# Kernel tuning notes

Hardware: AMD Instinct MI355X
Metric: run time of the kernel (lower is better)

## Reference

```python
import jax, jax.numpy as jnp
import numpy as np

EMB = 1024
HEADS = 16
HEAD = EMB // HEADS
B, S = 4, 1024


def setup_inputs() -> dict:
    key = jax.random.key(0)
    ks = jax.random.split(key, 8)
    glorot = lambda k, shp: jax.random.normal(k, shp, jnp.float32) * np.sqrt(2.0 / (shp[-2] + shp[-1]))
    return {
        "inputs_for_keys": jax.random.normal(ks[0], (B, S, EMB), jnp.float32),
        "inputs_for_values": jax.random.normal(ks[1], (B, S, EMB), jnp.float32),
        "inputs_for_queries": jax.random.normal(ks[2], (B, S, EMB), jnp.float32),
        "Wk": glorot(ks[3], (HEADS, EMB, HEAD)),
        "Wv": glorot(ks[4], (HEADS, EMB, HEAD)),
        "Wq": glorot(ks[5], (HEADS, EMB, HEAD)),
        "Wo": glorot(ks[6], (EMB, EMB)),
        "bo": jnp.zeros((EMB,), jnp.float32),
    }


def reference(inputs_for_keys, inputs_for_values, inputs_for_queries, Wk, Wv, Wq, Wo, bo):
    # Batched equivalent of the per-head loop: project all heads at once.
    K = jnp.einsum("bse,hed->bhsd", inputs_for_keys, Wk)
    V = jnp.einsum("bse,hed->bhsd", inputs_for_values, Wv)
    Q = jnp.einsum("bse,hed->bhsd", inputs_for_queries, Wq)
    s_keys = K.shape[2]
    s_q = Q.shape[2]
    # causal mask: -inf strictly above diagonal (original: np.triu(ones*-inf, k=1))
    mask = jnp.where(jnp.triu(jnp.ones((s_q, s_keys), bool), k=1), -jnp.inf, 0.0).astype(jnp.float32)
    logits = jnp.einsum("bhqd,bhkd->bhqk", Q, K)
    # FAITHFUL quirk: original divides (logits + mask) by sqrt(window_size_keys)
    scores = jax.nn.softmax((logits + mask) / np.sqrt(s_keys), axis=-1)
    ctx = jnp.einsum("bhqk,bhkd->bhqd", scores, V)  # [B,H,Sq,Dh]
    # concat heads along last dim (head order matches loop order)
    concat = ctx.transpose(0, 2, 1, 3).reshape(ctx.shape[0], s_q, -1)  # [B,Sq,E]
    return jax.nn.relu(concat @ Wo + bo)
```

## Files before the change

### kernel.cpp

```cpp
#include <hip/hip_runtime.h>
#include <hip/hip_bf16.h>

typedef unsigned short u16;
typedef unsigned int   u32;
typedef __attribute__((ext_vector_type(4))) float f32x4;
typedef __attribute__((ext_vector_type(8))) short bf16x8;

#define EMB   1024
#define SEQ   1024
#define HEADS 16
#define DH    64
#define BATCH 4
#define BH    64
#define BS    4096
#define LDP   72
#define NEG_BIG (-1.0e30f)

__device__ __forceinline__ float b2f(u16 u){ return __uint_as_float(((u32)u) << 16); }
__device__ __forceinline__ u16 f2b(float f){
    u32 u = __float_as_uint(f);
    u32 r = u + 0x7fffu + ((u >> 16) & 1u);
    return (u16)(r >> 16);
}
__device__ __forceinline__ void zero4(f32x4& v){ v[0]=0.f; v[1]=0.f; v[2]=0.f; v[3]=0.f; }
__device__ __forceinline__ ushort4 pk4(float a, float b, float c, float d){
    ushort4 p; p.x = f2b(a); p.y = f2b(b); p.z = f2b(c); p.w = f2b(d); return p;
}

__device__ __forceinline__ u16* tptr(u16* base, int row, int col ){
    const int phys = ((col >> 3) ^ (row & 7));
    return base + row * 64 + (phys << 3);
}

__device__ __forceinline__ void dot2_f32(const float* __restrict__ x,
                                         const float* __restrict__ w, const int ws,
                                         float& a0, float& a1)
{
    float s0 = 0.f, s1 = 0.f;
    for (int e = 0; e < EMB; e += 4) {
        const float4 xv = *(const float4*)(x + e);
        const float2 w0 = *(const float2*)(w + (size_t)(e + 0) * ws);
        const float2 w1 = *(const float2*)(w + (size_t)(e + 1) * ws);
        const float2 w2 = *(const float2*)(w + (size_t)(e + 2) * ws);
        const float2 w3 = *(const float2*)(w + (size_t)(e + 3) * ws);
        s0 += xv.x * w0.x; s1 += xv.x * w0.y;
        s0 += xv.y * w1.x; s1 += xv.y * w1.y;
        s0 += xv.z * w2.x; s1 += xv.z * w2.y;
        s0 += xv.w * w3.x; s1 += xv.w * w3.y;
    }
    a0 = s0; a1 = s1;
}


__global__ __launch_bounds__(256) void convert_x(
    const float* __restrict__ Xk, const float* __restrict__ Xv, const float* __restrict__ Xq,
    u16* __restrict__ XB)
{
    const int which = blockIdx.y;
    const float* __restrict__ src = (which == 0) ? Xk : (which == 1) ? Xv : Xq;
    const size_t off = (size_t)blockIdx.x * 1024 + threadIdx.x * 4;
    const float4 v = *(const float4*)(src + off);
    *(ushort4*)(XB + (size_t)which * 4194304 + off) = pk4(v.x, v.y, v.z, v.w);
}

__global__ __launch_bounds__(256) void transpose_w(
    const float* __restrict__ Wk, const float* __restrict__ Wv, const float* __restrict__ Wq,
    const float* __restrict__ Wo, u16* __restrict__ WT, u16* __restrict__ WoT)
{
    __shared__ u16 T[64][LDP];
    const int which = blockIdx.y;
    const int bx = blockIdx.x, t = threadIdx.x;

    if (which < 3) {
        const float* __restrict__ W = (which == 0) ? Wk : (which == 1) ? Wv : Wq;
        const int h = bx >> 4, e0 = (bx & 15) * 64;
        #pragma unroll
        for (int i = 0; i < 16; ++i) {
            const int idx = i * 256 + t;
            const int e = idx >> 6, d = idx & 63;
            T[d][e] = f2b(W[(size_t)h * (EMB * DH) + (size_t)(e0 + e) * DH + d]);
        }
        __syncthreads();
        u16* dstb = WT + (size_t)which * (EMB * EMB / 16) * 16;
        #pragma unroll
        for (int i = 0; i < 2; ++i) {
            const int idx = i * 256 + t;
            const int d = idx >> 3, e8 = (idx & 7) * 8;
            *(bf16x8*)(dstb + (size_t)(h * 64 + d) * EMB + e0 + e8) = *(const bf16x8*)&T[d][e8];
        }
    } else {
        const int j0 = (bx >> 4) * 64, e0 = (bx & 15) * 64;
        #pragma unroll
        for (int i = 0; i < 16; ++i) {
            const int idx = i * 256 + t;
            const int e = idx >> 6, d = idx & 63;
            T[d][e] = f2b(Wo[(size_t)(e0 + e) * EMB + j0 + d]);
        }
        __syncthreads();
        #pragma unroll
        for (int i = 0; i < 2; ++i) {
            const int idx = i * 256 + t;
            const int d = idx >> 3, e8 = (idx & 7) * 8;
            *(bf16x8*)(WoT + (size_t)(j0 + d) * EMB + e0 + e8) = *(const bf16x8*)&T[d][e8];
        }
    }
}

template<int MODE>
__global__ __launch_bounds__(256) void gemm128(
    const u16* __restrict__ XB, const u16* __restrict__ WT,
    u16* __restrict__ Qw, u16* __restrict__ Kw, u16* __restrict__ Vt,
    const float* __restrict__ bo, float* __restrict__ OUT)
{
    __shared__ u16 As[128 * 64];
    __shared__ u16 Bs[128 * 64];

    const int t = threadIdx.x;
    const int wave = t >> 6, lane = t & 63;
    const int quad = lane >> 4, l16 = lane & 15;
    const int wrow = wave >> 1, wcol = wave & 1;
    const int m0 = blockIdx.x * 128;
    const int n0 = blockIdx.y * 128;
    const int which = blockIdx.z;

    const u16* __restrict__ Ag = (MODE == 0) ? XB + (size_t)which * 4194304 : XB;
    const u16* __restrict__ Bg = (MODE == 0) ? WT + (size_t)which * 1048576 : WT;

    f32x4 acc[4][4];
    #pragma unroll
    for (int mi = 0; mi < 4; ++mi)
        #pragma unroll
        for (int ni = 0; ni < 4; ++ni) zero4(acc[mi][ni]);

    for (int k0 = 0; k0 < EMB; k0 += 64) {
        bf16x8 abuf[4], bbuf[4];
        #pragma unroll
        for (int i = 0; i < 4; ++i) {
            const int c = i * 256 + t;
            const int row = c >> 3, col8 = (c & 7) * 8;
            abuf[i] = *(const bf16x8*)(Ag + (size_t)(m0 + row) * EMB + k0 + col8);
            bbuf[i] = *(const bf16x8*)(Bg + (size_t)(n0 + row) * EMB + k0 + col8);
        }
        #pragma unroll
        for (int i = 0; i < 4; ++i) {
            const int c = i * 256 + t;
            const int row = c >> 3, col8 = (c & 7) * 8;
            *(bf16x8*)tptr(As, row, col8) = abuf[i];
            *(bf16x8*)tptr(Bs, row, col8) = bbuf[i];
        }
        __syncthreads();

        #pragma unroll
        for (int kb = 0; kb < 2; ++kb) {
            bf16x8 af[4], bf[4];
            #pragma unroll
            for (int mi = 0; mi < 4; ++mi)
                af[mi] = *(const bf16x8*)tptr(As, wrow * 64 + mi * 16 + l16, kb * 32 + quad * 8);
            #pragma unroll
            for (int ni = 0; ni < 4; ++ni)
                bf[ni] = *(const bf16x8*)tptr(Bs, wcol * 64 + ni * 16 + l16, kb * 32 + quad * 8);
            #pragma unroll
            for (int mi = 0; mi < 4; ++mi)
                #pragma unroll
                for (int ni = 0; ni < 4; ++ni)
                    acc[mi][ni] = __builtin_amdgcn_mfma_f32_16x16x32_bf16(af[mi], bf[ni], acc[mi][ni], 0, 0, 0);
        }
        __syncthreads();
    }

    #pragma unroll
    for (int mi = 0; mi < 4; ++mi) {
        const int r = m0 + wrow * 64 + mi * 16 + quad * 4;
        #pragma unroll
        for (int ni = 0; ni < 4; ++ni) {
            const int j = n0 + wcol * 64 + ni * 16 + l16;
            if (MODE == 1) {
                const float bias = bo[j];
                #pragma unroll
                for (int reg = 0; reg < 4; ++reg) {
                    float v = acc[mi][ni][reg] + bias;
                    if (v < 0.f) v = 0.f;
                    OUT[(size_t)(r + reg) * EMB + j] = v;
                }
            } else {
                const int h = j >> 6, d = j & 63;
                const int b = r >> 10, s = r & (SEQ - 1);
                const int bh = b * HEADS + h;
                if (which == 1) {
                    *(ushort4*)(Vt + ((size_t)bh * DH + d) * SEQ + s) =
                        pk4(acc[mi][ni][0], acc[mi][ni][1], acc[mi][ni][2], acc[mi][ni][3]);
                } else {
                    u16* dst = (which == 0) ? Kw : Qw;
                    #pragma unroll
                    for (int reg = 0; reg < 4; ++reg)
                        dst[((size_t)bh * SEQ + s + reg) * DH + d] = f2b(acc[mi][ni][reg]);
                }
            }
        }
    }
}


__global__ __launch_bounds__(256) void qkv_proj_mfma(
    const float* __restrict__ Xk, const float* __restrict__ Xv, const float* __restrict__ Xq,
    const float* __restrict__ Wk, const float* __restrict__ Wv, const float* __restrict__ Wq,
    u16* __restrict__ Kw, u16* __restrict__ Vw, u16* __restrict__ Qw)
{
    __shared__ u16 As[128][LDP];
    __shared__ u16 Bs[64][LDP];

    const int which = blockIdx.z;
    const float* __restrict__ X = (which == 0) ? Xk : (which == 1) ? Xv : Xq;
    const float* __restrict__ W = (which == 0) ? Wk : (which == 1) ? Wv : Wq;

    const int h    = blockIdx.y;
    const int m0   = blockIdx.x * 128;
    const int t    = threadIdx.x;
    const int wave = t >> 6, lane = t & 63;
    const int quad = lane >> 4, l16 = lane & 15;

    f32x4 acc[2][4];
    #pragma unroll
    for (int mi = 0; mi < 2; ++mi)
        #pragma unroll
        for (int ni = 0; ni < 4; ++ni) zero4(acc[mi][ni]);

    const size_t wbase = (size_t)h * EMB * DH;
    for (int k0 = 0; k0 < EMB; k0 += 64) {
        #pragma unroll
        for (int i = 0; i < 8; ++i) {
            const int idx = i * 256 + t;
            const int r = idx >> 4, c4 = (idx & 15) * 4;
            const float4 v = *(const float4*)(X + (size_t)(m0 + r) * EMB + k0 + c4);
            *(ushort4*)&As[r][c4] = pk4(v.x, v.y, v.z, v.w);
        }
        #pragma unroll
        for (int i = 0; i < 4; ++i) {
            const int d  = t & 63;
            const int e0 = (t >> 6) * 4 + i * 16;
            const float v0 = W[wbase + (size_t)(k0 + e0 + 0) * DH + d];
            const float v1 = W[wbase + (size_t)(k0 + e0 + 1) * DH + d];
            const float v2 = W[wbase + (size_t)(k0 + e0 + 2) * DH + d];
            const float v3 = W[wbase + (size_t)(k0 + e0 + 3) * DH + d];
            *(ushort4*)&Bs[d][e0] = pk4(v0, v1, v2, v3);
        }
        __syncthreads();

        #pragma unroll
        for (int kb = 0; kb < 2; ++kb) {
            bf16x8 bfr[4];
            #pragma unroll
            for (int ni = 0; ni < 4; ++ni)
                bfr[ni] = *(const bf16x8*)&Bs[ni * 16 + l16][kb * 32 + quad * 8];
            #pragma unroll
            for (int mi = 0; mi < 2; ++mi) {
                const bf16x8 af = *(const bf16x8*)&As[wave * 32 + mi * 16 + l16][kb * 32 + quad * 8];
                #pragma unroll
                for (int ni = 0; ni < 4; ++ni)
                    acc[mi][ni] = __builtin_amdgcn_mfma_f32_16x16x32_bf16(af, bfr[ni], acc[mi][ni], 0, 0, 0);
            }
        }
        __syncthreads();
    }

    const int b  = m0 >> 10;
    const int bh = b * HEADS + h;
    u16* __restrict__ RowDst = (which == 0) ? Kw : Qw;
    #pragma unroll
    for (int mi = 0; mi < 2; ++mi) {
        const int s_base = (m0 & (SEQ - 1)) + wave * 32 + mi * 16 + quad * 4;
        #pragma unroll
        for (int ni = 0; ni < 4; ++ni) {
            const int d = ni * 16 + l16;
            if (which != 1) {
                #pragma unroll
                for (int reg = 0; reg < 4; ++reg)
                    RowDst[((size_t)bh * SEQ + s_base + reg) * DH + d] = f2b(acc[mi][ni][reg]);
            } else {
                *(ushort4*)(Vw + ((size_t)bh * DH + d) * SEQ + s_base) =
                    pk4(acc[mi][ni][0], acc[mi][ni][1], acc[mi][ni][2], acc[mi][ni][3]);
            }
        }
    }
}

template<bool QWS, bool TOWS>
__global__ __launch_bounds__(256) void attn_flash(
    const float* __restrict__ Xq, const float* __restrict__ Wq,
    const u16* __restrict__ Qg, const u16* __restrict__ Kg, const u16* __restrict__ Vg,
    u16* __restrict__ CTXb, float* __restrict__ CTXf)
{
    __shared__ u16 Qs[64][LDP];
    union KVU {
        struct { u16 Ks[64][LDP]; u16 Vt[64][LDP]; } kv;
        struct { u16 Xs[64][LDP]; u16 WT[64][LDP]; } pr;
    };
    __shared__ KVU uu;
    __shared__ u16 Ps[64][LDP];

    const int t    = threadIdx.x;
    const int wave = t >> 6, lane = t & 63;
    const int quad = lane >> 4, l16 = lane & 15;
    const int qt = blockIdx.x, bh = blockIdx.y;
    const int b  = bh >> 4, h = bh & (HEADS - 1);
    const int q0 = qt * 64;

    if (QWS) {
        #pragma unroll
        for (int i = 0; i < 4; ++i) {
            const int idx = i * 256 + t;
            const int r = idx >> 4, c4 = (idx & 15) * 4;
            *(ushort4*)&Qs[r][c4] = *(const ushort4*)(Qg + ((size_t)bh * SEQ + q0 + r) * DH + c4);
        }
    } else {
        f32x4 qacc[4];
        #pragma unroll
        for (int ni = 0; ni < 4; ++ni) zero4(qacc[ni]);
        const size_t wbase = (size_t)h * EMB * DH;
        for (int k0 = 0; k0 < EMB; k0 += 64) {
            #pragma unroll
            for (int i = 0; i < 4; ++i) {
                const int idx = i * 256 + t;
                const int r = idx >> 4, c4 = (idx & 15) * 4;
                const float4 v = *(const float4*)(Xq + (size_t)(b * SEQ + q0 + r) * EMB + k0 + c4);
                *(ushort4*)&uu.pr.Xs[r][c4] = pk4(v.x, v.y, v.z, v.w);
            }
            #pragma unroll
            for (int i = 0; i < 4; ++i) {
                const int d  = t & 63;
                const int e0 = (t >> 6) * 4 + i * 16;
                const float v0 = Wq[wbase + (size_t)(k0 + e0 + 0) * DH + d];
                const float v1 = Wq[wbase + (size_t)(k0 + e0 + 1) * DH + d];
                const float v2 = Wq[wbase + (size_t)(k0 + e0 + 2) * DH + d];
                const float v3 = Wq[wbase + (size_t)(k0 + e0 + 3) * DH + d];
                *(ushort4*)&uu.pr.WT[d][e0] = pk4(v0, v1, v2, v3);
            }
            __syncthreads();
            #pragma unroll
            for (int kb = 0; kb < 2; ++kb) {
                const bf16x8 af = *(const bf16x8*)&uu.pr.Xs[wave * 16 + l16][kb * 32 + quad * 8];
                #pragma unroll
                for (int ni = 0; ni < 4; ++ni) {
                    const bf16x8 bf = *(const bf16x8*)&uu.pr.WT[ni * 16 + l16][kb * 32 + quad * 8];
                    qacc[ni] = __builtin_amdgcn_mfma_f32_16x16x32_bf16(af, bf, qacc[ni], 0, 0, 0);
                }
            }
            __syncthreads();
        }
        #pragma unroll
        for (int ni = 0; ni < 4; ++ni)
            #pragma unroll
            for (int reg = 0; reg < 4; ++reg)
                Qs[wave * 16 + quad * 4 + reg][ni * 16 + l16] = f2b(qacc[ni][reg]);
    }

    float m[4], l[4];
    #pragma unroll
    for (int reg = 0; reg < 4; ++reg) { m[reg] = NEG_BIG; l[reg] = 0.f; }
    f32x4 oacc[4];
    #pragma unroll
    for (int ni = 0; ni < 4; ++ni) zero4(oacc[ni]);
    __syncthreads();

    for (int c = 0; c <= qt; ++c) {
        const int k0 = c * 64;

        #pragma unroll
        for (int i = 0; i < 4; ++i) {
            const int idx = i * 256 + t;
            const int r = idx >> 4, c4 = (idx & 15) * 4;
            *(ushort4*)&uu.kv.Ks[r][c4] = *(const ushort4*)(Kg + ((size_t)bh * SEQ + k0 + r) * DH + c4);
        }
        #pragma unroll
        for (int i = 0; i < 4; ++i) {
            const int idx = i * 256 + t;
            const int r = idx >> 4, c4 = (idx & 15) * 4;
            *(ushort4*)&uu.kv.Vt[r][c4] = *(const ushort4*)(Vg + ((size_t)bh * DH + r) * SEQ + k0 + c4);
        }
        __syncthreads();

        f32x4 sacc[4];
        #pragma unroll
        for (int ni = 0; ni < 4; ++ni) zero4(sacc[ni]);
        #pragma unroll
        for (int kb = 0; kb < 2; ++kb) {
            const bf16x8 af = *(const bf16x8*)&Qs[wave * 16 + l16][kb * 32 + quad * 8];
            #pragma unroll
            for (int ni = 0; ni < 4; ++ni) {
                const bf16x8 bf = *(const bf16x8*)&uu.kv.Ks[ni * 16 + l16][kb * 32 + quad * 8];
                sacc[ni] = __builtin_amdgcn_mfma_f32_16x16x32_bf16(af, bf, sacc[ni], 0, 0, 0);
            }
        }

        const bool diag = (c == qt);
        #pragma unroll
        for (int reg = 0; reg < 4; ++reg) {
            const int rloc = quad * 4 + reg;
            float sv[4];
            #pragma unroll
            for (int ni = 0; ni < 4; ++ni) {
                float s = sacc[ni][reg] * 0.03125f;
                if (diag && (ni * 16 + l16 > wave * 16 + rloc)) s = NEG_BIG;
                sv[ni] = s;
            }
            float mx = fmaxf(fmaxf(sv[0], sv[1]), fmaxf(sv[2], sv[3]));
            mx = fmaxf(mx, m[reg]);
            #pragma unroll
            for (int off = 1; off < 16; off <<= 1) mx = fmaxf(mx, __shfl_xor(mx, off));
            const float alpha = __expf(m[reg] - mx);
            float rs = 0.f;
            #pragma unroll
            for (int ni = 0; ni < 4; ++ni) {
                const float p = __expf(sv[ni] - mx);
                Ps[wave * 16 + rloc][ni * 16 + l16] = f2b(p);
                rs += p;
            }
            #pragma unroll
            for (int off = 1; off < 16; off <<= 1) rs += __shfl_xor(rs, off);
            l[reg] = l[reg] * alpha + rs;
            m[reg] = mx;
            #pragma unroll
            for (int ni = 0; ni < 4; ++ni) oacc[ni][reg] *= alpha;
        }
        __syncthreads();

        #pragma unroll
        for (int kb = 0; kb < 2; ++kb) {
            const bf16x8 af = *(const bf16x8*)&Ps[wave * 16 + l16][kb * 32 + quad * 8];
            #pragma unroll
            for (int ni = 0; ni < 4; ++ni) {
                const bf16x8 bf = *(const bf16x8*)&uu.kv.Vt[ni * 16 + l16][kb * 32 + quad * 8];
                oacc[ni] = __builtin_amdgcn_mfma_f32_16x16x32_bf16(af, bf, oacc[ni], 0, 0, 0);
            }
        }
        __syncthreads();
    }

    float il[4];
    #pragma unroll
    for (int reg = 0; reg < 4; ++reg) il[reg] = 1.f / l[reg];
    #pragma unroll
    for (int ni = 0; ni < 4; ++ni) {
        const int d = ni * 16 + l16;
        #pragma unroll
        for (int reg = 0; reg < 4; ++reg) {
            const int q = wave * 16 + quad * 4 + reg;
            const float val = oacc[ni][reg] * il[reg];
            const size_t off = ((size_t)(b * SEQ + q0 + q)) * EMB + h * DH + d;
            if (TOWS) CTXb[off] = f2b(val);
            else      CTXf[off] = val;
        }
    }
}

__global__ __launch_bounds__(256) void out_proj_mfma(
    const u16* __restrict__ CTXb, const float* __restrict__ Wo,
    const float* __restrict__ bo, float* __restrict__ OUT)
{
    __shared__ u16 As[128][LDP];
    __shared__ u16 Bs[64][LDP];

    const int m0 = blockIdx.x * 128;
    const int n0 = blockIdx.y * 64;
    const int t = threadIdx.x;
    const int wave = t >> 6, lane = t & 63;
    const int quad = lane >> 4, l16 = lane & 15;

    f32x4 acc[2][4];
    #pragma unroll
    for (int mi = 0; mi < 2; ++mi)
        #pragma unroll
        for (int ni = 0; ni < 4; ++ni) zero4(acc[mi][ni]);

    for (int k0 = 0; k0 < EMB; k0 += 64) {
        #pragma unroll
        for (int i = 0; i < 8; ++i) {
            const int idx = i * 256 + t;
            const int r = idx >> 4, c4 = (idx & 15) * 4;
            *(ushort4*)&As[r][c4] = *(const ushort4*)(CTXb + (size_t)(m0 + r) * EMB + k0 + c4);
        }
        #pragma unroll
        for (int i = 0; i < 4; ++i) {
            const int d  = t & 63;
            const int e0 = (t >> 6) * 4 + i * 16;
            const float v0 = Wo[(size_t)(k0 + e0 + 0) * EMB + n0 + d];
            const float v1 = Wo[(size_t)(k0 + e0 + 1) * EMB + n0 + d];
            const float v2 = Wo[(size_t)(k0 + e0 + 2) * EMB + n0 + d];
            const float v3 = Wo[(size_t)(k0 + e0 + 3) * EMB + n0 + d];
            *(ushort4*)&Bs[d][e0] = pk4(v0, v1, v2, v3);
        }
        __syncthreads();
        #pragma unroll
        for (int kb = 0; kb < 2; ++kb) {
            bf16x8 bfr[4];
            #pragma unroll
            for (int ni = 0; ni < 4; ++ni)
                bfr[ni] = *(const bf16x8*)&Bs[ni * 16 + l16][kb * 32 + quad * 8];
            #pragma unroll
            for (int mi = 0; mi < 2; ++mi) {
                const bf16x8 af = *(const bf16x8*)&As[wave * 32 + mi * 16 + l16][kb * 32 + quad * 8];
                #pragma unroll
                for (int ni = 0; ni < 4; ++ni)
                    acc[mi][ni] = __builtin_amdgcn_mfma_f32_16x16x32_bf16(af, bfr[ni], acc[mi][ni], 0, 0, 0);
            }
        }
        __syncthreads();
    }

    #pragma unroll
    for (int mi = 0; mi < 2; ++mi) {
        const int row = m0 + wave * 32 + mi * 16 + quad * 4;
        #pragma unroll
        for (int ni = 0; ni < 4; ++ni) {
            const int col = n0 + ni * 16 + l16;
            const float bias = bo[col];
            #pragma unroll
            for (int reg = 0; reg < 4; ++reg) {
                float v = acc[mi][ni][reg] + bias;
                if (v < 0.f) v = 0.f;
                OUT[(size_t)(row + reg) * EMB + col] = v;
            }
        }
    }
}

__global__ __launch_bounds__(256) void out_proj_inplace(
    float* __restrict__ OUT, const float* __restrict__ Wo, const float* __restrict__ bo)
{
    __shared__ float Xs[8][EMB];
    const int t    = threadIdx.x;
    const int row0 = blockIdx.x * 8;
    {
        const float4* src = (const float4*)(OUT + (size_t)row0 * EMB);
        float4* dst = (float4*)&Xs[0][0];
        #pragma unroll
        for (int i = 0; i < 8; ++i) dst[i * 256 + t] = src[i * 256 + t];
    }
    __syncthreads();
    const int r  = t >> 5;
    const int j0 = (t & 31) * 2;
    const float* xrow = Xs[r];
    for (int jb = 0; jb < 16; ++jb) {
        const int j = jb * 64 + j0;
        float a0, a1;
        dot2_f32(xrow, Wo + j, EMB, a0, a1);
        a0 += bo[j];     if (a0 < 0.f) a0 = 0.f;
        a1 += bo[j + 1]; if (a1 < 0.f) a1 = 0.f;
        float* op = OUT + (size_t)(row0 + r) * EMB + j;
        op[0] = a0; op[1] = a1;
    }
}

extern "C" void kernel_launch(void* const* d_in, const int* in_sizes, int n_in,
                              void* d_out, int out_size, void* d_ws, size_t ws_size,
                              hipStream_t stream)
{
    const float* Xk = (const float*)d_in[0];
    const float* Xv = (const float*)d_in[1];
    const float* Xq = (const float*)d_in[2];
    const float* Wk = (const float*)d_in[3];
    const float* Wv = (const float*)d_in[4];
    const float* Wq = (const float*)d_in[5];
    const float* Wo = (const float*)d_in[6];
    const float* bo = (const float*)d_in[7];
    float* OUT = (float*)d_out;
    (void)in_sizes; (void)n_in; (void)out_size;

    const size_t SEGE = (size_t)BH * SEQ * DH;
    const size_t SEGB = SEGE * sizeof(u16);

    const size_t XB_OFF  = 0;
    const size_t WT_OFF  = 3 * SEGE;
    const size_t WOT_OFF = WT_OFF + 3 * (EMB * EMB / 64) * 64;
    const size_t QW_OFF  = WOT_OFF + (size_t)EMB * EMB;
    const size_t KW_OFF  = QW_OFF + SEGE;
    const size_t VT_OFF  = KW_OFF + SEGE;
    const size_t TIER_A_BYTES = (VT_OFF + SEGE) * sizeof(u16);

    if (ws_size >= TIER_A_BYTES) {
        u16* W16 = (u16*)d_ws;
        u16* XB  = W16 + XB_OFF;
        u16* WT  = W16 + WT_OFF;
        u16* WoT = W16 + WOT_OFF;
        u16* Qw  = W16 + QW_OFF;
        u16* Kw  = W16 + KW_OFF;
        u16* Vt  = W16 + VT_OFF;
        u16* CTX = XB;

        convert_x<<<dim3(4096, 3), 256, 0, stream>>>(Xk, Xv, Xq, XB);
        transpose_w<<<dim3(256, 4), 256, 0, stream>>>(Wk, Wv, Wq, Wo, WT, WoT);
        gemm128<0><<<dim3(32, 8, 3), 256, 0, stream>>>(XB, WT, Qw, Kw, Vt, nullptr, nullptr);
        attn_flash<true, true><<<dim3(SEQ / 64, BH), 256, 0, stream>>>(
            Xq, Wq, Qw, Kw, Vt, CTX, nullptr);
        gemm128<1><<<dim3(32, 8, 1), 256, 0, stream>>>(CTX, WoT, nullptr, nullptr, nullptr, bo, OUT);
    } else if (ws_size >= 4 * SEGB) {
        u16* Qw = (u16*)d_ws;
        u16* Kw = Qw + SEGE;
        u16* Vw = Kw + SEGE;
        u16* CT = Vw + SEGE;
        qkv_proj_mfma<<<dim3(32, HEADS, 3), 256, 0, stream>>>(Xk, Xv, Xq, Wk, Wv, Wq, Kw, Vw, Qw);
        attn_flash<true, true><<<dim3(SEQ / 64, BH), 256, 0, stream>>>(
            Xq, Wq, Qw, Kw, Vw, CT, nullptr);
        out_proj_mfma<<<dim3(32, EMB / 64), 256, 0, stream>>>(CT, Wo, bo, OUT);
    } else if (ws_size >= 3 * SEGB) {
        u16* Kw = (u16*)d_ws;
        u16* Vw = Kw + SEGE;
        u16* CT = Vw + SEGE;
        qkv_proj_mfma<<<dim3(32, HEADS, 2), 256, 0, stream>>>(Xk, Xv, Xq, Wk, Wv, Wq, Kw, Vw, nullptr);
        attn_flash<false, true><<<dim3(SEQ / 64, BH), 256, 0, stream>>>(
            Xq, Wq, nullptr, Kw, Vw, CT, nullptr);
        out_proj_mfma<<<dim3(32, EMB / 64), 256, 0, stream>>>(CT, Wo, bo, OUT);
    } else {
        u16* Kw = (u16*)d_ws;
        u16* Vw = Kw + SEGE;
        qkv_proj_mfma<<<dim3(32, HEADS, 2), 256, 0, stream>>>(Xk, Xv, Xq, Wk, Wv, Wq, Kw, Vw, nullptr);
        attn_flash<false, false><<<dim3(SEQ / 64, BH), 256, 0, stream>>>(
            Xq, Wq, nullptr, Kw, Vw, nullptr, OUT);
        out_proj_inplace<<<dim3(BS / 8), 256, 0, stream>>>(OUT, Wo, bo);
    }
}
```

Baseline: 240.1 us.

## Add register-prefetched double-buffered flash attention kernel with prescaled Q

Replaces the attention kernel on the main path with a new flash kernel. It keeps Q fragments in registers, double-buffers the K/V tiles in LDS with register prefetch of the next tile, and computes S^T with 16x16x32 MFMAs. It also staggers the query-tile order to balance causal work across blocks. The 1/sqrt(1024) softmax scale is folded into Q at projection time, and s_setprio hints are added around the MFMA sections. One barrier per tile is used, and more registers are held for the prefetch.

```diff
diff --git a/kernel.cpp b/kernel.cpp
--- a/kernel.cpp
+++ b/kernel.cpp
@@ -5,6 +5,7 @@
 typedef unsigned int   u32;
 typedef __attribute__((ext_vector_type(4))) float f32x4;
 typedef __attribute__((ext_vector_type(8))) short bf16x8;
+typedef __attribute__((ext_vector_type(4))) short bf16x4;
 
 #define EMB   1024
 #define SEQ   1024
@@ -30,6 +31,14 @@
 __device__ __forceinline__ u16* tptr(u16* base, int row, int col ){
     const int phys = ((col >> 3) ^ (row & 7));
     return base + row * 64 + (phys << 3);
+}
+__device__ __forceinline__ const u16* tptrc(const u16* base, int row, int col ){
+    const int phys = ((col >> 3) ^ (row & 7));
+    return base + row * 64 + (phys << 3);
+}
+__device__ __forceinline__ const u16* tptr8c(const u16* base, int row, int col ){
+    const int chunk = ((col >> 3) ^ (row & 7));
+    return base + row * 64 + (chunk << 3) + (col & 7);
 }
 
 __device__ __forceinline__ void dot2_f32(const float* __restrict__ x,
@@ -191,11 +200,160 @@
                         pk4(acc[mi][ni][0], acc[mi][ni][1], acc[mi][ni][2], acc[mi][ni][3]);
                 } else {
                     u16* dst = (which == 0) ? Kw : Qw;
+                    const float qsc = (which == 2) ? 0.03125f : 1.0f;
                     #pragma unroll
                     for (int reg = 0; reg < 4; ++reg)
-                        dst[((size_t)bh * SEQ + s + reg) * DH + d] = f2b(acc[mi][ni][reg]);
+                        dst[((size_t)bh * SEQ + s + reg) * DH + d] = f2b(acc[mi][ni][reg] * qsc);
                 }
             }
+        }
+    }
+}
+
+__global__ __launch_bounds__(256) void attn_flash2(
+    const u16* __restrict__ Qg, const u16* __restrict__ Kg, const u16* __restrict__ Vg,
+    u16* __restrict__ CTXb)
+{
+    __shared__ u16 Ks[2][64 * 64];
+    __shared__ u16 Vs[2][64 * 64];
+
+    const int t = threadIdx.x;
+    const int wave = t >> 6, lane = t & 63;
+    const int quad = lane >> 4, l16 = lane & 15;
+    const int bh = blockIdx.y;
+    const int qt = (blockIdx.x + (blockIdx.y >> 2)) & 15;
+    const int b = bh >> 4, h = bh & (HEADS - 1);
+    const int q0 = qt * 64;
+
+    const u16* __restrict__ Kbase = Kg + (size_t)bh * SEQ * DH;
+    const u16* __restrict__ Vbase = Vg + (size_t)bh * DH * SEQ;
+
+    bf16x8 qf[2];
+    {
+        const u16* qrow = Qg + ((size_t)bh * SEQ + q0 + wave * 16 + l16) * DH;
+        qf[0] = *(const bf16x8*)(qrow + quad * 8);
+        qf[1] = *(const bf16x8*)(qrow + 32 + quad * 8);
+    }
+
+    #pragma unroll
+    for (int i = 0; i < 2; ++i) {
+        const int c = i * 256 + t;
+        const int row = c >> 3, col8 = (c & 7) * 8;
+        const bf16x8 kv = *(const bf16x8*)(Kbase + (size_t)row * DH + col8);
+        const bf16x8 vv = *(const bf16x8*)(Vbase + (size_t)row * SEQ + col8);
+        *(bf16x8*)tptr(&Ks[0][0], row, col8) = kv;
+        *(bf16x8*)tptr(&Vs[0][0], row, col8) = vv;
+    }
+
+    float m = NEG_BIG, l = 0.f;
+    f32x4 oacc[4];
+    #pragma unroll
+    for (int nd = 0; nd < 4; ++nd) zero4(oacc[nd]);
+
+    __syncthreads();
+
+    const int qin = wave * 16 + l16;
+    int cur = 0;
+    for (int c = 0; c <= qt; ++c) {
+        const int kn = ((c < qt) ? c + 1 : qt) * 64;
+        bf16x8 kpre[2], vpre[2];
+        #pragma unroll
+        for (int i = 0; i < 2; ++i) {
+            const int cc = i * 256 + t;
+            const int row = cc >> 3, col8 = (cc & 7) * 8;
+            kpre[i] = *(const bf16x8*)(Kbase + (size_t)(kn + row) * DH + col8);
+            vpre[i] = *(const bf16x8*)(Vbase + (size_t)row * SEQ + kn + col8);
+        }
+
+        const u16* Kc = &Ks[cur][0];
+        const u16* Vc = &Vs[cur][0];
+
+        f32x4 sacc[4];
+        #pragma unroll
+        for (int ni = 0; ni < 4; ++ni) zero4(sacc[ni]);
+        __builtin_amdgcn_s_setprio(1);
+        #pragma unroll
+        for (int kb = 0; kb < 2; ++kb) {
+            #pragma unroll
+            for (int ni = 0; ni < 4; ++ni) {
+                const bf16x8 kf = *(const bf16x8*)tptrc(Kc, ni * 16 + l16, kb * 32 + quad * 8);
+                sacc[ni] = __builtin_amdgcn_mfma_f32_16x16x32_bf16(kf, qf[kb], sacc[ni], 0, 0, 0);
+            }
+        }
+        __builtin_amdgcn_s_setprio(0);
+
+        const bool diag = (c == qt);
+        float mx = m;
+        #pragma unroll
+        for (int ni = 0; ni < 4; ++ni) {
+            #pragma unroll
+            for (int reg = 0; reg < 4; ++reg) {
+                float s = sacc[ni][reg];
+                if (diag && (ni * 16 + quad * 4 + reg > qin)) s = NEG_BIG;
+                sacc[ni][reg] = s;
+                mx = fmaxf(mx, s);
+            }
+        }
+        mx = fmaxf(mx, __shfl_xor(mx, 16));
+        mx = fmaxf(mx, __shfl_xor(mx, 32));
+        const float alpha = __expf(m - mx);
+        m = mx;
+        float rs = 0.f;
+        bf16x4 pa[4];
+        #pragma unroll
+        for (int ni = 0; ni < 4; ++ni) {
+            const float p0 = __expf(sacc[ni][0] - mx);
+            const float p1 = __expf(sacc[ni][1] - mx);
+            const float p2 = __expf(sacc[ni][2] - mx);
+            const float p3 = __expf(sacc[ni][3] - mx);
+            rs += (p0 + p1) + (p2 + p3);
+            bf16x4 pk;
+            pk[0] = (short)f2b(p0); pk[1] = (short)f2b(p1);
+            pk[2] = (short)f2b(p2); pk[3] = (short)f2b(p3);
+            pa[ni] = pk;
+        }
+        rs += __shfl_xor(rs, 16);
+        rs += __shfl_xor(rs, 32);
+        l = l * alpha + rs;
+
+        #pragma unroll
+        for (int reg = 0; reg < 4; ++reg) {
+            const float ar = __shfl(alpha, quad * 4 + reg);
+            #pragma unroll
+            for (int nd = 0; nd < 4; ++nd) oacc[nd][reg] *= ar;
+        }
+
+        __builtin_amdgcn_s_setprio(1);
+        #pragma unroll
+        for (int ks = 0; ks < 4; ++ks) {
+            #pragma unroll
+            for (int nd = 0; nd < 4; ++nd) {
+                const bf16x4 vf = *(const bf16x4*)tptr8c(Vc, nd * 16 + l16, ks * 16 + quad * 4);
+                oacc[nd] = __builtin_amdgcn_mfma_f32_16x16x16bf16_1k(pa[ks], vf, oacc[nd], 0, 0, 0);
+            }
+        }
+        __builtin_amdgcn_s_setprio(0);
+
+        const int nxt = cur ^ 1;
+        #pragma unroll
+        for (int i = 0; i < 2; ++i) {
+            const int cc = i * 256 + t;
+            const int row = cc >> 3, col8 = (cc & 7) * 8;
+            *(bf16x8*)tptr(&Ks[nxt][0], row, col8) = kpre[i];
+            *(bf16x8*)tptr(&Vs[nxt][0], row, col8) = vpre[i];
+        }
+        __syncthreads();
+        cur = nxt;
+    }
+
+    #pragma unroll
+    for (int reg = 0; reg < 4; ++reg) {
+        const float il = 1.f / __shfl(l, quad * 4 + reg);
+        const int q = q0 + wave * 16 + quad * 4 + reg;
+        #pragma unroll
+        for (int nd = 0; nd < 4; ++nd) {
+            const int d = nd * 16 + l16;
+            CTXb[(size_t)(b * SEQ + q) * EMB + h * DH + d] = f2b(oacc[nd][reg] * il);
         }
     }
 }
@@ -590,8 +748,7 @@
         convert_x<<<dim3(4096, 3), 256, 0, stream>>>(Xk, Xv, Xq, XB);
         transpose_w<<<dim3(256, 4), 256, 0, stream>>>(Wk, Wv, Wq, Wo, WT, WoT);
         gemm128<0><<<dim3(32, 8, 3), 256, 0, stream>>>(XB, WT, Qw, Kw, Vt, nullptr, nullptr);
-        attn_flash<true, true><<<dim3(SEQ / 64, BH), 256, 0, stream>>>(
-            Xq, Wq, Qw, Kw, Vt, CTX, nullptr);
+        attn_flash2<<<dim3(SEQ / 64, BH), 256, 0, stream>>>(Qw, Kw, Vt, CTX);
         gemm128<1><<<dim3(32, 8, 1), 256, 0, stream>>>(CTX, WoT, nullptr, nullptr, nullptr, bo, OUT);
     } else if (ws_size >= 4 * SEGB) {
         u16* Qw = (u16*)d_ws;
```

Result: faster. 214.9 us (-10.5%).
